# Kernel tuning notes

Measured on AMD Instinct MI355X. Metric: run time of the kernel, lower is better.

The kernel has to match this reference:

```python
import jax, jax.numpy as jnp
import numpy as np

B, N, M = 4, 8192, 8192


def setup_inputs() -> dict:
    key = jax.random.key(0)
    k1, k2 = jax.random.split(key)
    xyz1 = jax.random.normal(k1, (B, N, 3), dtype=jnp.float32)
    xyz2 = jax.random.normal(k2, (B, M, 3), dtype=jnp.float32)
    return {"xyz1": xyz1, "xyz2": xyz2}


def _chamfer(xyz1, xyz2):
    # Squared Euclidean pairwise distances via the expansion
    # ||a-b||^2 = ||a||^2 + ||b||^2 - 2 a.b  (avoids a [B,N,M,3] diff tensor).
    sq1 = jnp.sum(xyz1 * xyz1, axis=-1)              # [B,N]
    sq2 = jnp.sum(xyz2 * xyz2, axis=-1)              # [B,M]
    inner = jnp.einsum('bnd,bmd->bnm', xyz1, xyz2)   # [B,N,M]
    d = sq1[:, :, None] + sq2[:, None, :] - 2.0 * inner
    d = jnp.maximum(d, 0.0)
    dist1 = jnp.min(d, axis=2)  # [B,N] nearest xyz2 point for each xyz1 point
    dist2 = jnp.min(d, axis=1)  # [B,M] nearest xyz1 point for each xyz2 point
    return dist1, dist2


def reference(xyz1, xyz2):
    return _chamfer(xyz1, xyz2)
```

## Files before the change

### kernel.cpp

```cpp
#include <hip/hip_runtime.h>


typedef __bf16 bf16_t;
typedef __bf16 bf16x8 __attribute__((ext_vector_type(8)));
typedef float  f32x16 __attribute__((ext_vector_type(16)));

#define NPTS    8192
#define NB      4
#define NSETPTS (NB * NPTS)
#define TPB     256
#define WAVES   4
#define QPW     2
#define QC      (WAVES * QPW * 32)
#define SEGR    4
#define RC      (NPTS / SEGR)
#define RT      (RC / 32)

__global__ void chamfer_init_out(unsigned int* __restrict__ out, int n) {
    int i = blockIdx.x * blockDim.x + threadIdx.x;
    if (i < n) out[i] = 0x7F800000u;
}

__device__ __forceinline__ void split2(float v, bf16_t& h, bf16_t& l) {
    h = (bf16_t)v;
    l = (bf16_t)(v - (float)h);
}

__global__ void chamfer_prep(const float* __restrict__ xyz1,
                             const float* __restrict__ xyz2,
                             bf16_t* __restrict__ a16,
                             bf16_t* __restrict__ b16) {
    int i = blockIdx.x * blockDim.x + threadIdx.x;
    const float* src = (i >= NSETPTS) ? xyz2 : xyz1;
    int p = i & (NSETPTS - 1);
    float x = src[3 * p], y = src[3 * p + 1], z = src[3 * p + 2];
    float sq = x * x + y * y + z * z;

    bf16_t m2xh, m2xl, m2yh, m2yl, m2zh, m2zl;
    split2(-2.f * x, m2xh, m2xl);
    split2(-2.f * y, m2yh, m2yl);
    split2(-2.f * z, m2zh, m2zl);
    bf16_t xh, xl, yh, yl, zh, zl;
    split2(x, xh, xl); split2(y, yh, yl); split2(z, zh, zl);
    bf16_t sqh, sql;
    split2(sq, sqh, sql);
    bf16_t one = (bf16_t)1.0f, zero = (bf16_t)0.0f;

    bf16_t A[16]  = { m2xh, m2yh, m2zh,  m2xl, m2yl, m2zl,
                      m2xh, m2yh, m2zh,  sqh, sql, one, one, zero, zero, zero };
    bf16_t Bv[16] = { xh, yh, zh,  xh, yh, zh,  xl, yl, zl,
                      one, one, sqh, sql, zero, zero, zero };

    const int perm[16] = {0,1,2,3, 8,9,10,11, 4,5,6,7, 12,13,14,15};
    bf16_t* ao = a16 + (size_t)i * 16;
    bf16_t* bo = b16 + (size_t)i * 16;
#pragma unroll
    for (int j = 0; j < 16; ++j) { ao[j] = A[perm[j]]; bo[j] = Bv[perm[j]]; }
}

__global__ __launch_bounds__(TPB, 4) void chamfer_main(
    const bf16_t* __restrict__ a16,
    const bf16_t* __restrict__ b16,
    unsigned int* __restrict__ out)
{
    __shared__ float red[WAVES][QPW][32][33];

    int bid = blockIdx.x;
    int s   = bid & (SEGR - 1); bid >>= 2;
    int qp  = bid & 31;         bid >>= 5;
    int b   = bid & 3;          bid >>= 2;
    int dir = bid;

    int wave = threadIdx.x >> 6;
    int lane = threadIdx.x & 63;
    int col  = lane & 31;
    int h    = lane >> 5;

    const bf16_t* ap = a16 + ((size_t)dir * NB + b) * NPTS * 16;
    const bf16_t* bp = b16 + ((size_t)(1 - dir) * NB + b) * NPTS * 16;

    int qbase = qp * QC + wave * (QPW * 32);
    const bf16x8* a0p = (const bf16x8*)(ap + (size_t)(qbase + col) * 16) + h;
    const bf16x8* a1p = (const bf16x8*)(ap + (size_t)(qbase + 32 + col) * 16) + h;
    bf16x8 af0 = *a0p;
    bf16x8 af1 = *a1p;

    int rbase = s * RC;
    const bf16x8* bptr = (const bf16x8*)(bp + (size_t)(rbase + col) * 16) + h;

    f32x16 rm0, rm1, zacc;
#pragma unroll
    for (int g = 0; g < 16; ++g) { rm0[g] = INFINITY; rm1[g] = INFINITY; zacc[g] = 0.f; }

    bf16x8 c0 = bptr[0];
    bf16x8 c1 = bptr[64];
    for (int t = 0; t < RT; t += 2) {
        int n0 = (t + 2 < RT) ? (t + 2) : t;
        int n1 = (t + 3 < RT) ? (t + 3) : (t + 1);
        bf16x8 p0 = bptr[(size_t)n0 * 64];
        bf16x8 p1 = bptr[(size_t)n1 * 64];

        f32x16 a0 = __builtin_amdgcn_mfma_f32_32x32x16_bf16(af0, c0, zacc, 0, 0, 0);
        f32x16 a1 = __builtin_amdgcn_mfma_f32_32x32x16_bf16(af0, c1, zacc, 0, 0, 0);
#pragma unroll
        for (int g = 0; g < 16; ++g)
            rm0[g] = fminf(fminf(a0[g], a1[g]), rm0[g]);

        f32x16 a2 = __builtin_amdgcn_mfma_f32_32x32x16_bf16(af1, c0, zacc, 0, 0, 0);
        f32x16 a3 = __builtin_amdgcn_mfma_f32_32x32x16_bf16(af1, c1, zacc, 0, 0, 0);
#pragma unroll
        for (int g = 0; g < 16; ++g)
            rm1[g] = fminf(fminf(a2[g], a3[g]), rm1[g]);

        c0 = p0;
        c1 = p1;
    }

#pragma unroll
    for (int g = 0; g < 16; ++g) {
        int row = (g & 3) + 8 * (g >> 2) + 4 * h;
        red[wave][0][row][col] = rm0[g];
        red[wave][1][row][col] = rm1[g];
    }
    __syncthreads();

    {
        int w   = threadIdx.x >> 6;
        int rem = threadIdx.x & 63;
        int qt  = rem >> 5;
        int r   = rem & 31;
        const float* rp = &red[w][qt][r][0];
        float v0 = rp[0], v1 = rp[1], v2 = rp[2], v3 = rp[3];
#pragma unroll
        for (int c = 4; c < 32; c += 4) {
            v0 = fminf(v0, rp[c + 0]);
            v1 = fminf(v1, rp[c + 1]);
            v2 = fminf(v2, rp[c + 2]);
            v3 = fminf(v3, rp[c + 3]);
        }
        float v = fmaxf(fminf(fminf(v0, v1), fminf(v2, v3)), 0.f);
        unsigned idx = (unsigned)(dir * NSETPTS + b * NPTS + qp * QC + threadIdx.x);
        atomicMin(&out[idx], __float_as_uint(v));
    }
}

extern "C" void kernel_launch(void* const* d_in, const int* in_sizes, int n_in,
                              void* d_out, int out_size, void* d_ws, size_t ws_size,
                              hipStream_t stream) {
    const float* xyz1 = (const float*)d_in[0];
    const float* xyz2 = (const float*)d_in[1];
    unsigned int* out = (unsigned int*)d_out;

    bf16_t* a16 = (bf16_t*)d_ws;
    bf16_t* b16 = a16 + (size_t)2 * NSETPTS * 16;

    hipLaunchKernelGGL(chamfer_init_out,
                       dim3((out_size + TPB - 1) / TPB), dim3(TPB), 0, stream,
                       out, out_size);

    hipLaunchKernelGGL(chamfer_prep,
                       dim3(2 * NSETPTS / TPB), dim3(TPB), 0, stream,
                       xyz1, xyz2, a16, b16);

    hipLaunchKernelGGL(chamfer_main,
                       dim3(2 * NB * (NPTS / QC) * SEGR), dim3(TPB), 0, stream,
                       a16, b16, out);
}
```

Before: 77.76 us.

## Use one query tile per wave, halve row segments, prefetch two tiles ahead

Each wave now owns a single 32-query tile instead of two, and the reference set is split into two segments instead of four. The grid size stays the same, but each block scans twice as many reference points. The reference-tile prefetch is deepened to two iterations ahead with extra registers. This lowers accumulator register use and halves the number of atomicMin writes per query, but each loaded B fragment now feeds half as many MFMAs, so L1/L2 load traffic per unit of compute roughly doubles.

```diff
diff --git a/kernel.cpp b/kernel.cpp
--- a/kernel.cpp
+++ b/kernel.cpp
@@ -10,9 +10,9 @@
 #define NSETPTS (NB * NPTS)
 #define TPB     256
 #define WAVES   4
-#define QPW     2
-#define QC      (WAVES * QPW * 32)
-#define SEGR    4
+#define QC      (WAVES * 32)
+#define QPANELS (NPTS / QC)
+#define SEGR    2
 #define RC      (NPTS / SEGR)
 #define RT      (RC / 32)
 
@@ -63,12 +63,12 @@
     const bf16_t* __restrict__ b16,
     unsigned int* __restrict__ out)
 {
-    __shared__ float red[WAVES][QPW][32][33];
+    __shared__ float red[WAVES][32][33];
 
     int bid = blockIdx.x;
-    int s   = bid & (SEGR - 1); bid >>= 2;
-    int qp  = bid & 31;         bid >>= 5;
-    int b   = bid & 3;          bid >>= 2;
+    int s   = bid & (SEGR - 1);    bid >>= 1;
+    int qp  = bid & (QPANELS - 1); bid >>= 6;
+    int b   = bid & 3;             bid >>= 2;
     int dir = bid;
 
     int wave = threadIdx.x >> 6;
@@ -79,57 +79,46 @@
     const bf16_t* ap = a16 + ((size_t)dir * NB + b) * NPTS * 16;
     const bf16_t* bp = b16 + ((size_t)(1 - dir) * NB + b) * NPTS * 16;
 
-    int qbase = qp * QC + wave * (QPW * 32);
-    const bf16x8* a0p = (const bf16x8*)(ap + (size_t)(qbase + col) * 16) + h;
-    const bf16x8* a1p = (const bf16x8*)(ap + (size_t)(qbase + 32 + col) * 16) + h;
-    bf16x8 af0 = *a0p;
-    bf16x8 af1 = *a1p;
+    int qbase = qp * QC + wave * 32;
+    bf16x8 af = *((const bf16x8*)(ap + (size_t)(qbase + col) * 16) + h);
 
-    int rbase = s * RC;
-    const bf16x8* bptr = (const bf16x8*)(bp + (size_t)(rbase + col) * 16) + h;
+    const bf16x8* bptr = (const bf16x8*)(bp + (size_t)(s * RC) * 16) + h;
+    const bf16x8* bl = bptr + col * 2;
 
-    f32x16 rm0, rm1, zacc;
+    f32x16 rm, zacc;
 #pragma unroll
-    for (int g = 0; g < 16; ++g) { rm0[g] = INFINITY; rm1[g] = INFINITY; zacc[g] = 0.f; }
+    for (int g = 0; g < 16; ++g) { rm[g] = INFINITY; zacc[g] = 0.f; }
 
-    bf16x8 c0 = bptr[0];
-    bf16x8 c1 = bptr[64];
+    bf16x8 c0 = bl[0 * 64];
+    bf16x8 c1 = bl[1 * 64];
+    bf16x8 d0 = bl[2 * 64];
+    bf16x8 d1 = bl[3 * 64];
     for (int t = 0; t < RT; t += 2) {
-        int n0 = (t + 2 < RT) ? (t + 2) : t;
-        int n1 = (t + 3 < RT) ? (t + 3) : (t + 1);
-        bf16x8 p0 = bptr[(size_t)n0 * 64];
-        bf16x8 p1 = bptr[(size_t)n1 * 64];
+        int n0 = (t + 4 < RT) ? (t + 4) : 0;
+        int n1 = (t + 5 < RT) ? (t + 5) : 0;
+        bf16x8 p0 = bl[(size_t)n0 * 64];
+        bf16x8 p1 = bl[(size_t)n1 * 64];
 
-        f32x16 a0 = __builtin_amdgcn_mfma_f32_32x32x16_bf16(af0, c0, zacc, 0, 0, 0);
-        f32x16 a1 = __builtin_amdgcn_mfma_f32_32x32x16_bf16(af0, c1, zacc, 0, 0, 0);
+        f32x16 a0 = __builtin_amdgcn_mfma_f32_32x32x16_bf16(af, c0, zacc, 0, 0, 0);
+        f32x16 a1 = __builtin_amdgcn_mfma_f32_32x32x16_bf16(af, c1, zacc, 0, 0, 0);
 #pragma unroll
         for (int g = 0; g < 16; ++g)
-            rm0[g] = fminf(fminf(a0[g], a1[g]), rm0[g]);
+            rm[g] = fminf(fminf(a0[g], a1[g]), rm[g]);
 
-        f32x16 a2 = __builtin_amdgcn_mfma_f32_32x32x16_bf16(af1, c0, zacc, 0, 0, 0);
-        f32x16 a3 = __builtin_amdgcn_mfma_f32_32x32x16_bf16(af1, c1, zacc, 0, 0, 0);
-#pragma unroll
-        for (int g = 0; g < 16; ++g)
-            rm1[g] = fminf(fminf(a2[g], a3[g]), rm1[g]);
-
-        c0 = p0;
-        c1 = p1;
+        c0 = d0; c1 = d1;
+        d0 = p0; d1 = p1;
     }
 
 #pragma unroll
     for (int g = 0; g < 16; ++g) {
         int row = (g & 3) + 8 * (g >> 2) + 4 * h;
-        red[wave][0][row][col] = rm0[g];
-        red[wave][1][row][col] = rm1[g];
+        red[wave][row][col] = rm[g];
     }
     __syncthreads();
 
-    {
-        int w   = threadIdx.x >> 6;
-        int rem = threadIdx.x & 63;
-        int qt  = rem >> 5;
-        int r   = rem & 31;
-        const float* rp = &red[w][qt][r][0];
+    if (threadIdx.x < QC) {
+        int w = threadIdx.x >> 5, r = threadIdx.x & 31;
+        const float* rp = &red[w][r][0];
         float v0 = rp[0], v1 = rp[1], v2 = rp[2], v3 = rp[3];
 #pragma unroll
         for (int c = 4; c < 32; c += 4) {
@@ -163,6 +152,6 @@
                        xyz1, xyz2, a16, b16);
 
     hipLaunchKernelGGL(chamfer_main,
-                       dim3(2 * NB * (NPTS / QC) * SEGR), dim3(TPB), 0, stream,
+                       dim3(2 * NB * QPANELS * SEGR), dim3(TPB), 0, stream,
                        a16, b16, out);
 }
```

Measured after the change: 84.96 us. 9.3% more time.

## Stage reference tiles through LDS with double-buffered direct global-to-LDS loads

Applied to the files above, without the earlier changes.

Each block now loads its reference point fragments cooperatively into shared memory using global_load_lds, double-buffered in 8-tile chunks, instead of every wave reading B fragments straight from global memory into registers. The four waves in a block share each staged tile, so global/L2 traffic drops by about the wave count and load latency is overlapped with MFMA work on the other buffer. In exchange it adds a block-wide barrier per chunk and LDS reads, and it reuses the reduction buffer's memory for staging.

```diff
diff --git a/kernel.cpp b/kernel.cpp
--- a/kernel.cpp
+++ b/kernel.cpp
@@ -12,13 +12,23 @@
 #define WAVES   4
 #define QPW     2
 #define QC      (WAVES * QPW * 32)
+#define QPANELS (NPTS / QC)
 #define SEGR    4
 #define RC      (NPTS / SEGR)
 #define RT      (RC / 32)
+#define BUFTILES 8
+#define BUFBF   (BUFTILES * 32 * 16)
+#define NBUF    (RT / BUFTILES)
 
 __global__ void chamfer_init_out(unsigned int* __restrict__ out, int n) {
     int i = blockIdx.x * blockDim.x + threadIdx.x;
     if (i < n) out[i] = 0x7F800000u;
+}
+
+__device__ __forceinline__ void gload16(const bf16_t* g, bf16_t* l) {
+    __builtin_amdgcn_global_load_lds(
+        (const __attribute__((address_space(1))) void*)g,
+        (__attribute__((address_space(3))) void*)l, 16, 0, 0);
 }
 
 __device__ __forceinline__ void split2(float v, bf16_t& h, bf16_t& l) {
@@ -63,58 +73,67 @@
     const bf16_t* __restrict__ b16,
     unsigned int* __restrict__ out)
 {
-    __shared__ float red[WAVES][QPW][32][33];
+    __shared__ __align__(16) unsigned char smem[WAVES * QPW * 32 * 33 * 4];
+    bf16_t* sbuf = (bf16_t*)smem;
+    float (*red)[QPW][32][33] = (float (*)[QPW][32][33])smem;
 
     int bid = blockIdx.x;
-    int s   = bid & (SEGR - 1); bid >>= 2;
-    int qp  = bid & 31;         bid >>= 5;
-    int b   = bid & 3;          bid >>= 2;
+    int s   = bid & (SEGR - 1);    bid >>= 2;
+    int qp  = bid & (QPANELS - 1); bid >>= 5;
+    int b   = bid & 3;             bid >>= 2;
     int dir = bid;
 
     int wave = threadIdx.x >> 6;
     int lane = threadIdx.x & 63;
     int col  = lane & 31;
     int h    = lane >> 5;
+    int fragoff = col * 16 + h * 8;
 
     const bf16_t* ap = a16 + ((size_t)dir * NB + b) * NPTS * 16;
     const bf16_t* bp = b16 + ((size_t)(1 - dir) * NB + b) * NPTS * 16;
+    const bf16_t* gB = bp + (size_t)(s * RC) * 16;
 
     int qbase = qp * QC + wave * (QPW * 32);
-    const bf16x8* a0p = (const bf16x8*)(ap + (size_t)(qbase + col) * 16) + h;
-    const bf16x8* a1p = (const bf16x8*)(ap + (size_t)(qbase + 32 + col) * 16) + h;
-    bf16x8 af0 = *a0p;
-    bf16x8 af1 = *a1p;
-
-    int rbase = s * RC;
-    const bf16x8* bptr = (const bf16x8*)(bp + (size_t)(rbase + col) * 16) + h;
+    bf16x8 af0 = *((const bf16x8*)(ap + (size_t)(qbase + col) * 16) + h);
+    bf16x8 af1 = *((const bf16x8*)(ap + (size_t)(qbase + 32 + col) * 16) + h);
 
     f32x16 rm0, rm1, zacc;
 #pragma unroll
     for (int g = 0; g < 16; ++g) { rm0[g] = INFINITY; rm1[g] = INFINITY; zacc[g] = 0.f; }
 
-    bf16x8 c0 = bptr[0];
-    bf16x8 c1 = bptr[64];
-    for (int t = 0; t < RT; t += 2) {
-        int n0 = (t + 2 < RT) ? (t + 2) : t;
-        int n1 = (t + 3 < RT) ? (t + 3) : (t + 1);
-        bf16x8 p0 = bptr[(size_t)n0 * 64];
-        bf16x8 p1 = bptr[(size_t)n1 * 64];
+    gload16(gB + wave * 512 + lane * 8,       sbuf + wave * 512);
+    gload16(gB + (4 + wave) * 512 + lane * 8, sbuf + (4 + wave) * 512);
 
-        f32x16 a0 = __builtin_amdgcn_mfma_f32_32x32x16_bf16(af0, c0, zacc, 0, 0, 0);
-        f32x16 a1 = __builtin_amdgcn_mfma_f32_32x32x16_bf16(af0, c1, zacc, 0, 0, 0);
+    for (int bi = 0; bi < NBUF; ++bi) {
+        int cur = bi & 1;
+        __syncthreads();
+        if (bi + 1 < NBUF) {
+            const bf16_t* gn = gB + (size_t)(bi + 1) * BUFBF;
+            bf16_t* dn = sbuf + (cur ^ 1) * BUFBF;
+            gload16(gn + wave * 512 + lane * 8,       dn + wave * 512);
+            gload16(gn + (4 + wave) * 512 + lane * 8, dn + (4 + wave) * 512);
+        }
+        const bf16_t* sc = sbuf + cur * BUFBF;
 #pragma unroll
-        for (int g = 0; g < 16; ++g)
-            rm0[g] = fminf(fminf(a0[g], a1[g]), rm0[g]);
+        for (int pg = 0; pg < BUFTILES / 2; ++pg) {
+            bf16x8 c0 = *(const bf16x8*)(sc + (2 * pg + 0) * 512 + fragoff);
+            bf16x8 c1 = *(const bf16x8*)(sc + (2 * pg + 1) * 512 + fragoff);
 
-        f32x16 a2 = __builtin_amdgcn_mfma_f32_32x32x16_bf16(af1, c0, zacc, 0, 0, 0);
-        f32x16 a3 = __builtin_amdgcn_mfma_f32_32x32x16_bf16(af1, c1, zacc, 0, 0, 0);
+            f32x16 a0 = __builtin_amdgcn_mfma_f32_32x32x16_bf16(af0, c0, zacc, 0, 0, 0);
+            f32x16 a1 = __builtin_amdgcn_mfma_f32_32x32x16_bf16(af0, c1, zacc, 0, 0, 0);
 #pragma unroll
-        for (int g = 0; g < 16; ++g)
-            rm1[g] = fminf(fminf(a2[g], a3[g]), rm1[g]);
+            for (int g = 0; g < 16; ++g)
+                rm0[g] = fminf(fminf(a0[g], a1[g]), rm0[g]);
 
-        c0 = p0;
-        c1 = p1;
+            f32x16 a2 = __builtin_amdgcn_mfma_f32_32x32x16_bf16(af1, c0, zacc, 0, 0, 0);
+            f32x16 a3 = __builtin_amdgcn_mfma_f32_32x32x16_bf16(af1, c1, zacc, 0, 0, 0);
+#pragma unroll
+            for (int g = 0; g < 16; ++g)
+                rm1[g] = fminf(fminf(a2[g], a3[g]), rm1[g]);
+        }
     }
+
+    __syncthreads();
 
 #pragma unroll
     for (int g = 0; g < 16; ++g) {
@@ -163,6 +182,6 @@
                        xyz1, xyz2, a16, b16);
 
     hipLaunchKernelGGL(chamfer_main,
-                       dim3(2 * NB * (NPTS / QC) * SEGR), dim3(TPB), 0, stream,
+                       dim3(2 * NB * QPANELS * SEGR), dim3(TPB), 0, stream,
                        a16, b16, out);
 }
```

Result: slower. 112.9 us (+45.2%).
